# Kernel optimization log

Measured on AMD Instinct MI355X. Metric: run time of the kernel, lower is better.

## Reference

```python
import jax, jax.numpy as jnp
import numpy as np

FEAT = 1024
N_TAR = 60000
N_MSG = 45000


def setup_inputs() -> dict:
    key = jax.random.key(0)
    ks = jax.random.split(key, 8)
    s = 1.0 / np.sqrt(FEAT)  # torch Linear default init scale
    return {
        "msg_from_o": jax.random.normal(ks[0], (N_MSG, FEAT), jnp.float32),
        "msg_from_s": jax.random.normal(ks[1], (N_MSG, FEAT), jnp.float32),
        "o_ava_idx": jnp.arange(N_MSG, dtype=jnp.int32),
        "s_ava_idx": jnp.arange(N_MSG, dtype=jnp.int32),
        "tar_feat": jax.random.normal(ks[2], (N_TAR, FEAT), jnp.float32),
        "w1_W": jax.random.uniform(ks[3], (FEAT, FEAT), jnp.float32, -s, s),
        "w1_b": jax.random.uniform(ks[4], (FEAT,), jnp.float32, -s, s),
        "w2_W": jax.random.uniform(ks[5], (FEAT, FEAT), jnp.float32, -s, s),
        "w2_b": jax.random.uniform(ks[6], (FEAT,), jnp.float32, -s, s),
    }


def reference(msg_from_o, msg_from_s, o_ava_idx, s_ava_idx, tar_feat,
              w1_W, w1_b, w2_W, w2_b):
    # scatter messages into zero-padded [N_tar, F] tensors (apply_method='mean')
    padded_o = jnp.zeros_like(tar_feat).at[o_ava_idx].set(msg_from_o)
    padded_s = jnp.zeros_like(tar_feat).at[s_ava_idx].set(msg_from_s)
    summarized = (padded_o + padded_s) * 0.5
    # MassageApply: hidden = ReLU(Linear(msg)) + ReLU(Linear(tar)); out = msg + hidden
    hidden = jax.nn.relu(summarized @ w1_W.T + w1_b) \
           + jax.nn.relu(tar_feat @ w2_W.T + w2_b)
    return summarized + hidden
```

## Files before the change

kernel.cpp:

```cpp
#include <hip/hip_runtime.h>
#include <hip/hip_bf16.h>

#define FEAT 1024
#define NTAR 60000
#define NMSG 45000
#define MPAD 60032
#define BM 256
#define BN 256
#define BK 64
#define KT16 (FEAT / BK)
#define MTILES ((NTAR + BM - 1) / BM)
#define NTILES (FEAT / BN)
#define NWG (MTILES * NTILES)

typedef __bf16 bf16_t;
typedef __attribute__((ext_vector_type(8))) __bf16 bf16x8;
typedef __attribute__((ext_vector_type(4))) __bf16 bf16x4;
typedef __attribute__((ext_vector_type(4))) float f32x4;

#define BAR() asm volatile("s_barrier" ::: "memory")

__global__ __launch_bounds__(256) void build_inv_kernel(
    const int* __restrict__ o_idx, const int* __restrict__ s_idx,
    int* __restrict__ inv_o, int* __restrict__ inv_s, int n) {
  int i = blockIdx.x * 256 + threadIdx.x;
  if (i < n) {
    inv_o[o_idx[i]] = i;
    inv_s[s_idx[i]] = i;
  }
}

__global__ __launch_bounds__(256) void convw_kernel(
    const float* __restrict__ w1, const float* __restrict__ w2,
    bf16_t* __restrict__ W1b, bf16_t* __restrict__ W2b) {
  int i = (blockIdx.x * 256 + threadIdx.x) * 4;
  f32x4 v1 = *(const f32x4*)(w1 + i);
  f32x4 v2 = *(const f32x4*)(w2 + i);
  bf16x4 o1, o2;
#pragma unroll
  for (int j = 0; j < 4; ++j) {
    o1[j] = (bf16_t)v1[j];
    o2[j] = (bf16_t)v2[j];
  }
  *(bf16x4*)(W1b + i) = o1;
  *(bf16x4*)(W2b + i) = o2;
}

__global__ __launch_bounds__(256) void prep_kernel(
    const float* __restrict__ msg_o, const float* __restrict__ msg_s,
    const float* __restrict__ tar,
    const int* __restrict__ inv_o, const int* __restrict__ inv_s,
    bf16_t* __restrict__ A1, bf16_t* __restrict__ A2) {
  const int total = MPAD * (FEAT / 4);
  const int stride = gridDim.x * 256;
#pragma unroll 2
  for (int e = blockIdx.x * 256 + threadIdx.x; e < total; e += stride) {
    const long r = e >> 8;
    const int c = (e & 255) * 4;
    bf16x4 s_out, t_out;
    if (r < NTAR) {
      const int mo = inv_o[r];
      const int ms = inv_s[r];
      f32x4 zed = {0.f, 0.f, 0.f, 0.f};
      f32x4 vo = (mo >= 0) ? *(const f32x4*)(msg_o + (long)mo * FEAT + c) : zed;
      f32x4 vs = (ms >= 0) ? *(const f32x4*)(msg_s + (long)ms * FEAT + c) : zed;
      f32x4 vt = *(const f32x4*)(tar + r * FEAT + c);
#pragma unroll
      for (int j = 0; j < 4; ++j) {
        s_out[j] = (bf16_t)(0.5f * (vo[j] + vs[j]));
        t_out[j] = (bf16_t)vt[j];
      }
    } else {
#pragma unroll
      for (int j = 0; j < 4; ++j) {
        s_out[j] = (bf16_t)0.f;
        t_out[j] = (bf16_t)0.f;
      }
    }
    *(bf16x4*)(A1 + r * FEAT + c) = s_out;
    *(bf16x4*)(A2 + r * FEAT + c) = t_out;
  }
}

template <bool FUSE_S>
__global__ __launch_bounds__(512, 2) void gemm8_kernel(
    const bf16_t* __restrict__ Ap, const bf16_t* __restrict__ Wp,
    const float* __restrict__ bias, const bf16_t* __restrict__ sS,
    float* __restrict__ out) {
  __shared__ char lds[131072];
  const int tid = threadIdx.x;
  const int lane = tid & 63;
  const int wid = tid >> 6;
  const int wm = wid >> 2;
  const int wn = wid & 3;
  const int g4 = lane >> 4;
  const int r16 = lane & 15;
  const int k7 = r16 & 7;
  const int cb0 = (g4 ^ k7) * 16;
  const int cb1 = ((4 + g4) ^ k7) * 16;

  const int orig = blockIdx.x;
  const int xcd = orig & 7, j = orig >> 3;
  const int wgid = (xcd < 4 ? xcd * 118 : 472 + (xcd - 4) * 117) + j;
  const int mtile = wgid >> 2;
  const int ntile = wgid & 3;
  const long row0 = (long)mtile * BM;
  const int col0 = ntile * BN;

  auto stageA = [&](int buf, int h, int kt) {
#pragma unroll
    for (int i = 0; i < 2; ++i) {
      const int idx = i * 512 + tid;
      const int rl = idx >> 3;
      const int row = (rl & 63) + ((rl >> 6) << 7) + (h << 6);
      const int gc = (idx & 7) ^ (rl & 7);
      const bf16_t* src = Ap + (row0 + row) * FEAT + kt * BK + gc * 8;
      __builtin_amdgcn_global_load_lds(
          (const __attribute__((address_space(1))) void*)src,
          (__attribute__((address_space(3))) void*)(lds + buf * 65536 +
                                                    h * 16384 + idx * 16),
          16, 0, 0);
    }
  };
  auto stageB = [&](int buf, int s, int kt) {
#pragma unroll
    for (int i = 0; i < 2; ++i) {
      const int idx = i * 512 + tid;
      const int rl = idx >> 3;
      const int row = (rl & 31) + ((rl >> 5) << 6) + (s << 5);
      const int gc = (idx & 7) ^ (rl & 7);
      const bf16_t* src = Wp + (long)(col0 + row) * FEAT + kt * BK + gc * 8;
      __builtin_amdgcn_global_load_lds(
          (const __attribute__((address_space(1))) void*)src,
          (__attribute__((address_space(3))) void*)(lds + buf * 65536 + 32768 +
                                                    s * 16384 + idx * 16),
          16, 0, 0);
    }
  };

  f32x4 acc[8][4] = {};
  bf16x8 a[4][2], b0[2][2], b1[2][2];

  auto loadA = [&](const char* L, int q) {
#pragma unroll
    for (int m2 = 0; m2 < 4; ++m2) {
      const char* p = L + q * 16384 + (wm * 64 + m2 * 16 + r16) * 128;
      a[m2][0] = *(const bf16x8*)(p + cb0);
      a[m2][1] = *(const bf16x8*)(p + cb1);
    }
  };
  auto loadB = [&](const char* L, int s, bf16x8(&b)[2][2]) {
#pragma unroll
    for (int nn = 0; nn < 2; ++nn) {
      const char* p = L + 32768 + s * 16384 + (wn * 32 + nn * 16 + r16) * 128;
      b[nn][0] = *(const bf16x8*)(p + cb0);
      b[nn][1] = *(const bf16x8*)(p + cb1);
    }
  };
  auto mfma16 = [&](int q, int s, bf16x8(&b)[2][2]) {
    __builtin_amdgcn_s_setprio(1);
#pragma unroll
    for (int m2 = 0; m2 < 4; ++m2)
#pragma unroll
      for (int nn = 0; nn < 2; ++nn)
#pragma unroll
        for (int kk = 0; kk < 2; ++kk)
          acc[q * 4 + m2][s * 2 + nn] = __builtin_amdgcn_mfma_f32_16x16x32_bf16(
              a[m2][kk], b[nn][kk], acc[q * 4 + m2][s * 2 + nn], 0, 0, 0);
    __builtin_amdgcn_s_setprio(0);
  };

  stageA(0, 0, 0); stageB(0, 0, 0); stageB(0, 1, 0); stageA(0, 1, 0);
  stageB(1, 0, 1); stageA(1, 0, 1);
  asm volatile("s_waitcnt vmcnt(4)" ::: "memory");
  BAR();
  loadB(lds, 0, b0);

  for (int kt = 0; kt < KT16; ++kt) {
    const int buf = kt & 1;
    const char* L = lds + buf * 65536;
    const char* Ln = lds + (buf ^ 1) * 65536;
    loadA(L, 0);
    if (kt + 1 < KT16) { stageB(buf ^ 1, 1, kt + 1); stageA(buf ^ 1, 1, kt + 1); }
    BAR();
    mfma16(0, 0, b0);
    loadB(L, 1, b1);
    if (kt + 2 < KT16) stageB(buf, 0, kt + 2);
    BAR();
    mfma16(0, 1, b1);
    loadA(L, 1);
    if (kt + 2 < KT16) stageA(buf, 0, kt + 2);
    BAR();
    mfma16(1, 0, b0);
    if (kt < KT16 - 2)
      asm volatile("s_waitcnt vmcnt(4)" ::: "memory");
    else
      asm volatile("s_waitcnt vmcnt(0)" ::: "memory");
    BAR();
    if (kt + 1 < KT16) loadB(Ln, 0, b0);
    mfma16(1, 1, b1);
  }

  float bv[4];
#pragma unroll
  for (int ni = 0; ni < 4; ++ni) bv[ni] = bias[col0 + wn * 64 + ni * 16 + r16];
#pragma unroll
  for (int mi = 0; mi < 8; ++mi) {
    const int q = mi >> 2, m2 = mi & 3;
#pragma unroll
    for (int r = 0; r < 4; ++r) {
      const long row = row0 + wm * 128 + q * 64 + m2 * 16 + g4 * 4 + r;
      if (row < NTAR) {
#pragma unroll
        for (int ni = 0; ni < 4; ++ni) {
          const int col = col0 + wn * 64 + ni * 16 + r16;
          float v = fmaxf(acc[mi][ni][r] + bv[ni], 0.f);
          if (FUSE_S) {
            v += (float)sS[row * FEAT + col];
            out[row * FEAT + col] = v;
          } else {
            out[row * FEAT + col] += v;
          }
        }
      }
    }
  }
}

extern "C" void kernel_launch(void* const* d_in, const int* in_sizes, int n_in,
                              void* d_out, int out_size, void* d_ws, size_t ws_size,
                              hipStream_t stream) {
  const float* msg_o = (const float*)d_in[0];
  const float* msg_s = (const float*)d_in[1];
  const int* o_idx = (const int*)d_in[2];
  const int* s_idx = (const int*)d_in[3];
  const float* tar = (const float*)d_in[4];
  const float* w1 = (const float*)d_in[5];
  const float* b1 = (const float*)d_in[6];
  const float* w2 = (const float*)d_in[7];
  const float* b2 = (const float*)d_in[8];
  float* out = (float*)d_out;

  char* ws = (char*)d_ws;
  bf16_t* A1 = (bf16_t*)ws;
  bf16_t* A2 = (bf16_t*)(ws + (size_t)MPAD * FEAT * 2);
  bf16_t* W1b = (bf16_t*)(ws + (size_t)MPAD * FEAT * 4);
  bf16_t* W2b = (bf16_t*)(ws + (size_t)MPAD * FEAT * 4 + (size_t)FEAT * FEAT * 2);
  int* inv_o = (int*)(ws + (size_t)MPAD * FEAT * 4 + (size_t)FEAT * FEAT * 4);
  int* inv_s = inv_o + MPAD;

  hipMemsetAsync(inv_o, 0xFF, (size_t)MPAD * 2 * sizeof(int), stream);
  build_inv_kernel<<<(NMSG + 255) / 256, 256, 0, stream>>>(o_idx, s_idx, inv_o,
                                                           inv_s, NMSG);
  convw_kernel<<<(FEAT * FEAT / 4) / 256, 256, 0, stream>>>(w1, w2, W1b, W2b);
  prep_kernel<<<4096, 256, 0, stream>>>(msg_o, msg_s, tar, inv_o, inv_s, A1, A2);
  gemm8_kernel<true><<<NWG, 512, 0, stream>>>(A1, W1b, b1, A1, out);
  gemm8_kernel<false><<<NWG, 512, 0, stream>>>(A2, W2b, b2, (const bf16_t*)nullptr, out);
}
```

Baseline: 1.003 ms.

## Precompute staging offsets, unroll GEMM k-loop by two, and reshuffle prefetch schedule

Hoists per-thread global and LDS address arithmetic for the async global-to-LDS staging and the LDS fragment loads out of the k-loop into precomputed offset arrays. The k-loop is manually unrolled by two with constant buffer indices so LDS base addresses fold to immediates. The B0 fragment load moves from the end of the previous iteration to the start of the current one, and the B0 staging for kt+2 is grouped with the A staging. The goal is fewer scalar/vector address instructions in the hot loop, at the cost of extra registers and a changed overlap between LDS reads and MFMA.

```diff
diff --git a/kernel.cpp b/kernel.cpp
--- a/kernel.cpp
+++ b/kernel.cpp
@@ -95,9 +95,7 @@
   const int wn = wid & 3;
   const int g4 = lane >> 4;
   const int r16 = lane & 15;
-  const int k7 = r16 & 7;
-  const int cb0 = (g4 ^ k7) * 16;
-  const int cb1 = ((4 + g4) ^ k7) * 16;
+  const int cb0 = ((g4 ^ (r16 & 7)) * 16);
 
   const int orig = blockIdx.x;
   const int xcd = orig & 7, j = orig >> 3;
@@ -107,36 +105,48 @@
   const long row0 = (long)mtile * BM;
   const int col0 = ntile * BN;
 
+  int offA[2][2], offB[2][2], dstOff[2];
+#pragma unroll
+  for (int i = 0; i < 2; ++i) {
+    const int idx = i * 512 + tid;
+    const int rl = idx >> 3;
+    const int gc = (idx & 7) ^ (rl & 7);
+    dstOff[i] = idx * 16;
+#pragma unroll
+    for (int h = 0; h < 2; ++h) {
+      offA[i][h] = ((rl & 63) + ((rl >> 6) << 7) + (h << 6)) * FEAT + gc * 8;
+      offB[i][h] = ((rl & 31) + ((rl >> 5) << 6) + (h << 5)) * FEAT + gc * 8;
+    }
+  }
+  const bf16_t* Abase = Ap + row0 * FEAT;
+  const bf16_t* Bbase = Wp + (long)col0 * FEAT;
+
   auto stageA = [&](int buf, int h, int kt) {
 #pragma unroll
-    for (int i = 0; i < 2; ++i) {
-      const int idx = i * 512 + tid;
-      const int rl = idx >> 3;
-      const int row = (rl & 63) + ((rl >> 6) << 7) + (h << 6);
-      const int gc = (idx & 7) ^ (rl & 7);
-      const bf16_t* src = Ap + (row0 + row) * FEAT + kt * BK + gc * 8;
+    for (int i = 0; i < 2; ++i)
       __builtin_amdgcn_global_load_lds(
-          (const __attribute__((address_space(1))) void*)src,
+          (const __attribute__((address_space(1))) void*)(Abase + kt * BK +
+                                                          offA[i][h]),
           (__attribute__((address_space(3))) void*)(lds + buf * 65536 +
-                                                    h * 16384 + idx * 16),
+                                                    h * 16384 + dstOff[i]),
           16, 0, 0);
-    }
   };
   auto stageB = [&](int buf, int s, int kt) {
 #pragma unroll
-    for (int i = 0; i < 2; ++i) {
-      const int idx = i * 512 + tid;
-      const int rl = idx >> 3;
-      const int row = (rl & 31) + ((rl >> 5) << 6) + (s << 5);
-      const int gc = (idx & 7) ^ (rl & 7);
-      const bf16_t* src = Wp + (long)(col0 + row) * FEAT + kt * BK + gc * 8;
+    for (int i = 0; i < 2; ++i)
       __builtin_amdgcn_global_load_lds(
-          (const __attribute__((address_space(1))) void*)src,
+          (const __attribute__((address_space(1))) void*)(Bbase + kt * BK +
+                                                          offB[i][s]),
           (__attribute__((address_space(3))) void*)(lds + buf * 65536 + 32768 +
-                                                    s * 16384 + idx * 16),
+                                                    s * 16384 + dstOff[i]),
           16, 0, 0);
-    }
-  };
+  };
+
+  int aOff[4], bOff[2];
+#pragma unroll
+  for (int m2 = 0; m2 < 4; ++m2) aOff[m2] = (wm * 64 + m2 * 16 + r16) * 128 + cb0;
+#pragma unroll
+  for (int nn = 0; nn < 2; ++nn) bOff[nn] = (wn * 32 + nn * 16 + r16) * 128 + cb0;
 
   f32x4 acc[8][4] = {};
   bf16x8 a[4][2], b0[2][2], b1[2][2];
@@ -144,17 +154,15 @@
   auto loadA = [&](const char* L, int q) {
 #pragma unroll
     for (int m2 = 0; m2 < 4; ++m2) {
-      const char* p = L + q * 16384 + (wm * 64 + m2 * 16 + r16) * 128;
-      a[m2][0] = *(const bf16x8*)(p + cb0);
-      a[m2][1] = *(const bf16x8*)(p + cb1);
+      a[m2][0] = *(const bf16x8*)(L + q * 16384 + aOff[m2]);
+      a[m2][1] = *(const bf16x8*)(L + q * 16384 + (aOff[m2] ^ 64));
     }
   };
   auto loadB = [&](const char* L, int s, bf16x8(&b)[2][2]) {
 #pragma unroll
     for (int nn = 0; nn < 2; ++nn) {
-      const char* p = L + 32768 + s * 16384 + (wn * 32 + nn * 16 + r16) * 128;
-      b[nn][0] = *(const bf16x8*)(p + cb0);
-      b[nn][1] = *(const bf16x8*)(p + cb1);
+      b[nn][0] = *(const bf16x8*)(L + 32768 + s * 16384 + bOff[nn]);
+      b[nn][1] = *(const bf16x8*)(L + 32768 + s * 16384 + (bOff[nn] ^ 64));
     }
   };
   auto mfma16 = [&](int q, int s, bf16x8(&b)[2][2]) {
@@ -170,26 +178,27 @@
     __builtin_amdgcn_s_setprio(0);
   };
 
+  float bv[4];
+#pragma unroll
+  for (int ni = 0; ni < 4; ++ni) bv[ni] = bias[col0 + wn * 64 + ni * 16 + r16];
+
   stageA(0, 0, 0); stageB(0, 0, 0); stageB(0, 1, 0); stageA(0, 1, 0);
   stageB(1, 0, 1); stageA(1, 0, 1);
   asm volatile("s_waitcnt vmcnt(4)" ::: "memory");
   BAR();
-  loadB(lds, 0, b0);
-
-  for (int kt = 0; kt < KT16; ++kt) {
-    const int buf = kt & 1;
+
+  auto body = [&](int kt, int buf) {
     const char* L = lds + buf * 65536;
-    const char* Ln = lds + (buf ^ 1) * 65536;
     loadA(L, 0);
+    loadB(L, 0, b0);
     if (kt + 1 < KT16) { stageB(buf ^ 1, 1, kt + 1); stageA(buf ^ 1, 1, kt + 1); }
     BAR();
     mfma16(0, 0, b0);
     loadB(L, 1, b1);
-    if (kt + 2 < KT16) stageB(buf, 0, kt + 2);
     BAR();
     mfma16(0, 1, b1);
     loadA(L, 1);
-    if (kt + 2 < KT16) stageA(buf, 0, kt + 2);
+    if (kt + 2 < KT16) { stageB(buf, 0, kt + 2); stageA(buf, 0, kt + 2); }
     BAR();
     mfma16(1, 0, b0);
     if (kt < KT16 - 2)
@@ -197,13 +206,14 @@
     else
       asm volatile("s_waitcnt vmcnt(0)" ::: "memory");
     BAR();
-    if (kt + 1 < KT16) loadB(Ln, 0, b0);
     mfma16(1, 1, b1);
-  }
-
-  float bv[4];
-#pragma unroll
-  for (int ni = 0; ni < 4; ++ni) bv[ni] = bias[col0 + wn * 64 + ni * 16 + r16];
+  };
+#pragma unroll 1
+  for (int kt = 0; kt < KT16; kt += 2) {
+    body(kt, 0);
+    body(kt + 1, 1);
+  }
+
 #pragma unroll
   for (int mi = 0; mi < 8; ++mi) {
     const int q = mi >> 2, m2 = mi & 3;
```

Result: no change. 1.004 ms (+0.1%).
